# Kernel optimization log

Measured on AMD Instinct MI355X. Metric: run time of the kernel, lower is better.

The kernel has to match this reference:

```python
import jax, jax.numpy as jnp
import numpy as np
from jax import lax

NUM_CLASSES = 21      # VOC: background (class 0) + 20 fg classes
TOP_K = 200           # max detections kept per (image, class)
CONF_THRESH = 0.01
NMS_THRESH = 0.45
VAR0, VAR1 = 0.1, 0.2 # cfg.VARIANCE
K_PRE = 256           # candidates pre-selected per class before NMS (fixed-shape NMS)


def setup_inputs() -> dict:
    key = jax.random.key(0)
    k1, k2, k3 = jax.random.split(key, 3)
    B, P, C = 32, 8732, NUM_CLASSES
    loc_data = jax.random.normal(k1, (B, P, 4), dtype=jnp.float32)
    conf_data = jax.random.normal(k2, (B, P, C), dtype=jnp.float32)
    u = jax.random.uniform(k3, (P, 4), dtype=jnp.float32)
    # priors in center-offset form: centers in [0,1), w/h in [0.02, 0.32)
    prior_data = jnp.concatenate([u[:, :2], 0.02 + 0.3 * u[:, 2:]], axis=-1)
    return {"loc_data": loc_data, "conf_data": conf_data, "prior_data": prior_data}


def decode(loc, priors):
    # loc, priors: [..., 4]; priors are (cx, cy, w, h)
    centers = priors[..., :2] + loc[..., :2] * VAR0 * priors[..., 2:]
    wh = priors[..., 2:] * jnp.exp(loc[..., 2:] * VAR1)
    xy_min = centers - wh * 0.5
    return jnp.concatenate([xy_min, xy_min + wh], axis=-1)  # (x1,y1,x2,y2)


def pairwise_iou(b):
    # b: [K, 4] corner boxes -> [K, K] IoU
    area = jnp.maximum(b[:, 2] - b[:, 0], 0.0) * jnp.maximum(b[:, 3] - b[:, 1], 0.0)
    lt = jnp.maximum(b[:, None, :2], b[None, :, :2])
    rb = jnp.minimum(b[:, None, 2:], b[None, :, 2:])
    wh = jnp.clip(rb - lt, 0.0)
    inter = wh[..., 0] * wh[..., 1]
    union = area[:, None] + area[None, :] - inter
    return inter / jnp.maximum(union, 1e-9)


def nms_one_class(scores_p, boxes_p4):
    # scores_p: [P], boxes_p4: [P, 4]; fixed-shape NMS -> [TOP_K, 5] (score, x1, y1, x2, y2)
    vals, idx = lax.top_k(scores_p, K_PRE)          # sorted descending
    cand = boxes_p4[idx]                            # [K_PRE, 4]
    valid = vals > CONF_THRESH
    iou = pairwise_iou(cand)                        # [K_PRE, K_PRE]
    ar = jnp.arange(K_PRE)

    def step(keep, i):
        # a kept box suppresses later boxes overlapping it above threshold
        sup = keep[i] & (iou[i] > NMS_THRESH) & (ar > i)
        return keep & (~sup), None

    keep, _ = lax.scan(step, valid, ar)
    kept_scores = jnp.where(keep, vals, 0.0)
    # kept entries are already score-ordered; pull the top TOP_K survivors to the front
    sv, si = lax.top_k(kept_scores, TOP_K)
    out_boxes = jnp.where(sv[:, None] > 0.0, cand[si], 0.0)
    return jnp.concatenate([sv[:, None], out_boxes], axis=-1)  # [TOP_K, 5]


def reference(loc_data, conf_data, prior_data):
    # loc_data: [B, P, 4], conf_data: [B, P, C], prior_data: [P, 4]
    probs = jax.nn.softmax(conf_data, axis=-1)                     # [B, P, C]
    probs_fg = jnp.swapaxes(probs[..., 1:], 1, 2)                  # [B, C-1, P] (skip background)
    boxes = decode(loc_data, prior_data[None, :, :])               # [B, P, 4]
    # vmap over classes, then over batch
    per_class = jax.vmap(nms_one_class, in_axes=(0, None))         # ([C-1,P],[P,4]) -> [C-1,TOP_K,5]
    per_image = jax.vmap(per_class, in_axes=(0, 0))
    return per_image(probs_fg, boxes)                              # [B, C-1, TOP_K, 5]
```

## Files before the change

kernel.cpp:

```cpp
#include <hip/hip_runtime.h>
#include <stdint.h>

typedef unsigned long long ull;

#define NUM_CLASSES 21
#define NFG 20
#define TOPK 200
#define KPRE 256
#define CONF_TH 0.01f
#define NMS_TH 0.45f
#define VAR0 0.1f
#define VAR1 0.2f
#define NVMAX 35
#define BITS_CONF 0x3C23D70Au
#define BITS_ONE1 0x3F800001u
#define BSLOT(g) ((g) + ((g) >> 6))

__global__ __launch_bounds__(256) void softmax_probs_kernel(
    const float* __restrict__ conf, float* __restrict__ probs, int P) {
    __shared__ __align__(16) float buf[256 * NUM_CLASSES];
    __shared__ __align__(16) float obuf[NFG * 256];
    const int t = threadIdx.x;
    const int b = blockIdx.y;
    const int p0 = blockIdx.x << 8;
    const int cnt = min(256, P - p0);
    const float* src = conf + ((size_t)b * P + p0) * NUM_CLASSES;

    if (cnt == 256) {
        const float4* s4 = (const float4*)src;
        float4* b4 = (float4*)buf;
#pragma unroll
        for (int k = 0; k < 6; ++k) {
            int i = (k << 8) + t;
            if (i < (256 * NUM_CLASSES) / 4) b4[i] = s4[i];
        }
    } else {
        int n = cnt * NUM_CLASSES;
        for (int i = t; i < n; i += 256) buf[i] = src[i];
    }
    __syncthreads();

    if (t < cnt) {
        const float* row = buf + t * NUM_CLASSES;
        float x[NUM_CLASSES];
        float mx = row[0];
        x[0] = mx;
#pragma unroll
        for (int j = 1; j < NUM_CLASSES; ++j) { x[j] = row[j]; mx = fmaxf(mx, x[j]); }
        float s = 0.f;
#pragma unroll
        for (int j = 0; j < NUM_CLASSES; ++j) { x[j] = expf(x[j] - mx); s += x[j]; }
#pragma unroll
        for (int c = 1; c < NUM_CLASSES; ++c)
            obuf[(c - 1) * 256 + t] = x[c] / s;
    }
    __syncthreads();

    float* dst = probs + ((size_t)b * NFG) * P + p0;
    if (cnt == 256) {
#pragma unroll
        for (int k = 0; k < 5; ++k) {
            int e = (k << 8) + t;
            int c = e >> 6;
            int f = e & 63;
            float4 val = ((const float4*)obuf)[(c << 6) + f];
            *(float4*)(dst + (size_t)c * P + (f << 2)) = val;
        }
    } else {
        for (int e = t; e < NFG * cnt; e += 256) {
            int c = e / cnt;
            int f = e - c * cnt;
            dst[(size_t)c * P + f] = obuf[c * 256 + f];
        }
    }
}

__global__ __launch_bounds__(KPRE) void nms_topk_kernel(
    const float* __restrict__ probs, const float* __restrict__ loc,
    const float* __restrict__ prior, float* __restrict__ out, int B, int P) {

    __shared__ ull arr[2 * KPRE];
    __shared__ ull arr2[2 * KPRE];
    __shared__ int wsum[2][4];
    __shared__ int s_cnt;
    __shared__ float4 sbox[KPRE + (KPRE >> 6)];
    __shared__ float sarea[KPRE + (KPRE >> 6)];
    __shared__ ull smask[KPRE][5];
    __shared__ ull kept_mask[4];

    const int t = threadIdx.x;
    const int lane = t & 63;
    const int wid = t >> 6;
    const ull lmask_lt = (1ULL << lane) - 1ULL;
    const int pair = blockIdx.x;
    const int b = pair / NFG;
    const float* sp = probs + (size_t)pair * P;

    unsigned int ubits[NVMAX];
#pragma unroll
    for (int i = 0; i < NVMAX; ++i) {
        int p = (i << 8) + t;
        ubits[i] = (p < P) ? __float_as_uint(sp[p]) : 0u;
    }

    {
        unsigned int lo = BITS_CONF, hi = BITS_ONE1;
        while (hi - lo > 1u) {
            unsigned int mid = lo + ((hi - lo) >> 1);
            int c = 0;
#pragma unroll
            for (int i = 0; i < NVMAX; ++i)
                c += __popcll(__ballot(ubits[i] >= mid));
            if (c >= KPRE / 4) lo = mid; else hi = mid;
        }
        if (lane == 0) wsum[0][wid] = (int)lo;
    }
    __syncthreads();
    unsigned int T = (unsigned int)min(min(wsum[0][0], wsum[0][1]),
                                       min(wsum[0][2], wsum[0][3]));

    int nval;
    for (int attempt = 0;; ++attempt) {
        if (t == 0) s_cnt = 0;
        __syncthreads();
        int wtot = 0;
#pragma unroll
        for (int i = 0; i < NVMAX; ++i) {
            int p = (i << 8) + t;
            bool pred = (p < P) && (ubits[i] >= T);
            wtot += __popcll(__ballot(pred));
        }
        int wbase = 0;
        if (lane == 0) wbase = atomicAdd(&s_cnt, wtot);
        wbase = __shfl(wbase, 0);
        int run = wbase;
#pragma unroll
        for (int i = 0; i < NVMAX; ++i) {
            int p = (i << 8) + t;
            bool pred = (p < P) && (ubits[i] >= T);
            ull bal = __ballot(pred);
            if (pred) {
                int slot = run + __popcll(bal & lmask_lt);
                if (slot < 2 * KPRE)
                    arr[slot] = ((ull)ubits[i] << 32) | (unsigned int)(~p);
            }
            run += __popcll(bal);
        }
        __syncthreads();
        if (s_cnt <= 2 * KPRE || attempt == 1) { nval = min(s_cnt, 2 * KPRE); break; }
        unsigned int lo = T, hi = BITS_ONE1;
        int it = 0;
        while (hi - lo > 1u) {
            unsigned int mid = lo + ((hi - lo) >> 1);
            int c = 0;
#pragma unroll
            for (int i = 0; i < NVMAX; ++i)
                c += __popcll(__ballot(ubits[i] >= mid));
            if (lane == 0) wsum[it & 1][wid] = c;
            __syncthreads();
            int totc = wsum[it & 1][0] + wsum[it & 1][1] + wsum[it & 1][2] + wsum[it & 1][3];
            if (totc >= KPRE) lo = mid; else hi = mid;
            ++it;
        }
        T = lo;
    }

    for (int e = t; e < 2 * KPRE; e += KPRE)
        if (e >= nval) arr[e] = 0ULL;
    __syncthreads();

    ull k0 = arr[t];
    ull k1 = arr[t + KPRE];
    {
        int lstage = 0;
#pragma unroll
        for (int kk = 2; kk <= 2 * KPRE; kk <<= 1) {
#pragma unroll
            for (int j = kk >> 1; j > 0; j >>= 1) {
                if (j == KPRE) {
                    ull mx = (k0 > k1) ? k0 : k1;
                    ull mn = (k0 > k1) ? k1 : k0;
                    k0 = mx; k1 = mn;
                } else if (j >= 64) {
                    ull* A = (lstage & 1) ? arr : arr2;
                    ++lstage;
                    A[t] = k0; A[t + KPRE] = k1;
                    __syncthreads();
                    ull o0 = A[t ^ j];
                    ull o1 = A[(t + KPRE) ^ j];
                    bool amLow = ((t & j) == 0);
                    bool d0 = ((t & kk) == 0);
                    bool d1 = (((t + KPRE) & kk) == 0);
                    k0 = (d0 == amLow) ? ((k0 > o0) ? k0 : o0) : ((k0 > o0) ? o0 : k0);
                    k1 = (d1 == amLow) ? ((k1 > o1) ? k1 : o1) : ((k1 > o1) ? o1 : k1);
                } else {
                    ull o0 = __shfl_xor(k0, j);
                    ull o1 = __shfl_xor(k1, j);
                    bool amLow = ((t & j) == 0);
                    bool d0 = ((t & kk) == 0);
                    bool d1 = (((t + KPRE) & kk) == 0);
                    k0 = (d0 == amLow) ? ((k0 > o0) ? k0 : o0) : ((k0 > o0) ? o0 : k0);
                    k1 = (d1 == amLow) ? ((k1 > o1) ? k1 : o1) : ((k1 > o1) ? o1 : k1);
                }
            }
        }
    }
    const ull key = k0;

    float v = __uint_as_float((unsigned int)(key >> 32));
    int idx = (int)(~(unsigned int)(key & 0xFFFFFFFFu));
    if (idx < 0 || idx >= P) { idx = 0; v = 0.f; }

    const float4 lv = *(const float4*)(loc + ((size_t)b * P + idx) * 4);
    const float4 pv = *(const float4*)(prior + (size_t)idx * 4);
    float cx = pv.x + (lv.x * VAR0) * pv.z;
    float cy = pv.y + (lv.y * VAR0) * pv.w;
    float w = pv.z * expf(lv.z * VAR1);
    float h = pv.w * expf(lv.w * VAR1);
    float x1 = cx - w * 0.5f;
    float y1 = cy - h * 0.5f;
    float x2 = x1 + w;
    float y2 = y1 + h;
    float myarea = fmaxf(x2 - x1, 0.f) * fmaxf(y2 - y1, 0.f);

    sbox[BSLOT(t)] = make_float4(x1, y1, x2, y2);
    sarea[BSLOT(t)] = myarea;
    __syncthreads();

#pragma unroll
    for (int rep = 0; rep < 3; ++rep) {
        int pid = t + (rep << 8);
        if (pid < 640) {
            int r, w2;
            if (pid < 64)       { r = pid;                w2 = 0; }
            else if (pid < 192) { int q = pid - 64;  r = 64  + (q >> 1); w2 = q & 1; }
            else if (pid < 384) { int q = pid - 192; int q3 = q / 3; r = 128 + q3; w2 = q - 3 * q3; }
            else                { int q = pid - 384; r = 192 + (q >> 2); w2 = q & 3; }
            float4 rb = sbox[BSLOT(r)];
            float ra = sarea[BSLOT(r)];
            ull mm = 0ULL;
            for (int i = 0; i < 64; ++i) {
                int g = (w2 << 6) + i;
                float4 gb = sbox[BSLOT(g)];
                float lx = fmaxf(gb.x, rb.x), ly = fmaxf(gb.y, rb.y);
                float rx = fminf(gb.z, rb.z), ry = fminf(gb.w, rb.w);
                float iw = fmaxf(rx - lx, 0.f), ih = fmaxf(ry - ly, 0.f);
                float inter = iw * ih;
                float uni = sarea[BSLOT(g)] + ra - inter;
                bool s = (inter / fmaxf(uni, 1e-9f)) > NMS_TH;
                mm |= ((ull)(s ? 1u : 0u)) << i;
            }
            smask[r][w2] = mm;
        }
    }
    __syncthreads();

    ull m0 = smask[t][0];
    ull m1 = (wid >= 1) ? smask[t][1] : 0ULL;
    ull m2 = (wid >= 2) ? smask[t][2] : 0ULL;
    ull m3 = (wid >= 3) ? smask[t][3] : 0ULL;
    if (wid == 0) m0 &= lmask_lt;
    else if (wid == 1) m1 &= lmask_lt;
    else if (wid == 2) m2 &= lmask_lt;
    else m3 &= lmask_lt;

    int alive = (v > CONF_TH) ? 1 : 0;
    ull mykept = 0ULL;
#pragma unroll
    for (int w2 = 0; w2 < 4; ++w2) {
        if (wid == w2) {
            if (w2 > 0 && (m0 & kept_mask[0])) alive = 0;
            if (w2 > 1 && (m1 & kept_mask[1])) alive = 0;
            if (w2 > 2 && (m2 & kept_mask[2])) alive = 0;
            ull mw = (w2 == 0) ? m0 : (w2 == 1) ? m1 : (w2 == 2) ? m2 : m3;
            ull validb = __ballot(alive != 0);
            ull todo = __ballot((mw & validb) != 0ULL) & validb;
            ull kept = validb & ~todo;
            while (todo) {
                int i = __builtin_ctzll(todo);
                ull row = __shfl(mw, i);
                if ((row & kept) == 0ULL) kept |= (1ULL << i);
                todo &= (todo - 1ULL);
            }
            mykept = kept;
            alive = (int)((kept >> lane) & 1ULL);
            if (lane == 0) kept_mask[w2] = kept;
        }
        __syncthreads();
    }

    int rank = 0;
#pragma unroll
    for (int w2 = 0; w2 < 4; ++w2)
        if (w2 < wid) rank += __popcll(kept_mask[w2]);
    rank += __popcll(mykept & lmask_lt);
    int total = 0;
#pragma unroll
    for (int w2 = 0; w2 < 4; ++w2) total += __popcll(kept_mask[w2]);

    float* orow = out + (size_t)pair * TOPK * 5;
    if (alive && rank < TOPK) {
        float* o = orow + rank * 5;
        o[0] = v; o[1] = x1; o[2] = y1; o[3] = x2; o[4] = y2;
    }
    if (t < TOPK && t >= total) {
        float* o = orow + t * 5;
        o[0] = 0.f; o[1] = 0.f; o[2] = 0.f; o[3] = 0.f; o[4] = 0.f;
    }
}

extern "C" void kernel_launch(void* const* d_in, const int* in_sizes, int n_in,
                              void* d_out, int out_size, void* d_ws, size_t ws_size,
                              hipStream_t stream) {
    const float* loc = (const float*)d_in[0];
    const float* conf = (const float*)d_in[1];
    const float* prior = (const float*)d_in[2];
    float* out = (float*)d_out;
    float* probs = (float*)d_ws;

    int P = in_sizes[2] / 4;
    int B = in_sizes[0] / (4 * P);

    dim3 g1((P + 255) / 256, B);
    softmax_probs_kernel<<<g1, 256, 0, stream>>>(conf, probs, P);
    nms_topk_kernel<<<B * NFG, KPRE, 0, stream>>>(probs, loc, prior, out, B, P);
}
```

Measured before the change: 137.5 us.

## Compute per-row softmax stats only and recompute probabilities inside NMS kernel

Measured after the change: 144.3 us. 1.05x slower.

```diff
diff --git a/kernel.cpp b/kernel.cpp
--- a/kernel.cpp
+++ b/kernel.cpp
@@ -16,10 +16,9 @@
 #define BITS_ONE1 0x3F800001u
 #define BSLOT(g) ((g) + ((g) >> 6))
 
-__global__ __launch_bounds__(256) void softmax_probs_kernel(
-    const float* __restrict__ conf, float* __restrict__ probs, int P) {
+__global__ __launch_bounds__(256) void rownorm_kernel(
+    const float* __restrict__ conf, float2* __restrict__ norm, int P) {
     __shared__ __align__(16) float buf[256 * NUM_CLASSES];
-    __shared__ __align__(16) float obuf[NFG * 256];
     const int t = threadIdx.x;
     const int b = blockIdx.y;
     const int p0 = blockIdx.x << 8;
@@ -49,35 +48,15 @@
         for (int j = 1; j < NUM_CLASSES; ++j) { x[j] = row[j]; mx = fmaxf(mx, x[j]); }
         float s = 0.f;
 #pragma unroll
-        for (int j = 0; j < NUM_CLASSES; ++j) { x[j] = expf(x[j] - mx); s += x[j]; }
-#pragma unroll
-        for (int c = 1; c < NUM_CLASSES; ++c)
-            obuf[(c - 1) * 256 + t] = x[c] / s;
-    }
-    __syncthreads();
-
-    float* dst = probs + ((size_t)b * NFG) * P + p0;
-    if (cnt == 256) {
-#pragma unroll
-        for (int k = 0; k < 5; ++k) {
-            int e = (k << 8) + t;
-            int c = e >> 6;
-            int f = e & 63;
-            float4 val = ((const float4*)obuf)[(c << 6) + f];
-            *(float4*)(dst + (size_t)c * P + (f << 2)) = val;
-        }
-    } else {
-        for (int e = t; e < NFG * cnt; e += 256) {
-            int c = e / cnt;
-            int f = e - c * cnt;
-            dst[(size_t)c * P + f] = obuf[c * 256 + f];
-        }
+        for (int j = 0; j < NUM_CLASSES; ++j) s += expf(x[j] - mx);
+        norm[(size_t)b * P + p0 + t] = make_float2(mx, s);
     }
 }
 
 __global__ __launch_bounds__(KPRE) void nms_topk_kernel(
-    const float* __restrict__ probs, const float* __restrict__ loc,
-    const float* __restrict__ prior, float* __restrict__ out, int B, int P) {
+    const float* __restrict__ conf, const float2* __restrict__ norm,
+    const float* __restrict__ loc, const float* __restrict__ prior,
+    float* __restrict__ out, int B, int P) {
 
     __shared__ ull arr[2 * KPRE];
     __shared__ ull arr2[2 * KPRE];
@@ -92,26 +71,43 @@
     const int lane = t & 63;
     const int wid = t >> 6;
     const ull lmask_lt = (1ULL << lane) - 1ULL;
-    const int pair = blockIdx.x;
-    const int b = pair / NFG;
-    const float* sp = probs + (size_t)pair * P;
+
+    const int g = blockIdx.x;
+    int b, c;
+    if ((B & 7) == 0) {
+        int k = g >> 3;
+        b = ((k / NFG) << 3) + (g & 7);
+        c = k - (k / NFG) * NFG;
+    } else {
+        b = g / NFG;
+        c = g - (g / NFG) * NFG;
+    }
+    const int pair = b * NFG + c;
+    const float* cb = conf + ((size_t)b * P) * NUM_CLASSES + (c + 1);
+    const float2* nb = norm + (size_t)b * P;
 
     unsigned int ubits[NVMAX];
 #pragma unroll
     for (int i = 0; i < NVMAX; ++i) {
         int p = (i << 8) + t;
-        ubits[i] = (p < P) ? __float_as_uint(sp[p]) : 0u;
+        if (p < P) {
+            float x = cb[(size_t)p * NUM_CLASSES];
+            float2 ms = nb[p];
+            ubits[i] = __float_as_uint(expf(x - ms.x) / ms.y);
+        } else {
+            ubits[i] = 0u;
+        }
     }
 
     {
         unsigned int lo = BITS_CONF, hi = BITS_ONE1;
         while (hi - lo > 1u) {
             unsigned int mid = lo + ((hi - lo) >> 1);
-            int c = 0;
+            int cc = 0;
 #pragma unroll
             for (int i = 0; i < NVMAX; ++i)
-                c += __popcll(__ballot(ubits[i] >= mid));
-            if (c >= KPRE / 4) lo = mid; else hi = mid;
+                cc += __popcll(__ballot(ubits[i] >= mid));
+            if (cc >= KPRE / 4) lo = mid; else hi = mid;
         }
         if (lane == 0) wsum[0][wid] = (int)lo;
     }
@@ -152,11 +148,11 @@
         int it = 0;
         while (hi - lo > 1u) {
             unsigned int mid = lo + ((hi - lo) >> 1);
-            int c = 0;
+            int cc = 0;
 #pragma unroll
             for (int i = 0; i < NVMAX; ++i)
-                c += __popcll(__ballot(ubits[i] >= mid));
-            if (lane == 0) wsum[it & 1][wid] = c;
+                cc += __popcll(__ballot(ubits[i] >= mid));
+            if (lane == 0) wsum[it & 1][wid] = cc;
             __syncthreads();
             int totc = wsum[it & 1][0] + wsum[it & 1][1] + wsum[it & 1][2] + wsum[it & 1][3];
             if (totc >= KPRE) lo = mid; else hi = mid;
@@ -240,13 +236,13 @@
             float ra = sarea[BSLOT(r)];
             ull mm = 0ULL;
             for (int i = 0; i < 64; ++i) {
-                int g = (w2 << 6) + i;
-                float4 gb = sbox[BSLOT(g)];
+                int gg = (w2 << 6) + i;
+                float4 gb = sbox[BSLOT(gg)];
                 float lx = fmaxf(gb.x, rb.x), ly = fmaxf(gb.y, rb.y);
                 float rx = fminf(gb.z, rb.z), ry = fminf(gb.w, rb.w);
                 float iw = fmaxf(rx - lx, 0.f), ih = fmaxf(ry - ly, 0.f);
                 float inter = iw * ih;
-                float uni = sarea[BSLOT(g)] + ra - inter;
+                float uni = sarea[BSLOT(gg)] + ra - inter;
                 bool s = (inter / fmaxf(uni, 1e-9f)) > NMS_TH;
                 mm |= ((ull)(s ? 1u : 0u)) << i;
             }
@@ -316,12 +312,12 @@
     const float* conf = (const float*)d_in[1];
     const float* prior = (const float*)d_in[2];
     float* out = (float*)d_out;
-    float* probs = (float*)d_ws;
+    float2* norm = (float2*)d_ws;
 
     int P = in_sizes[2] / 4;
     int B = in_sizes[0] / (4 * P);
 
     dim3 g1((P + 255) / 256, B);
-    softmax_probs_kernel<<<g1, 256, 0, stream>>>(conf, probs, P);
-    nms_topk_kernel<<<B * NFG, KPRE, 0, stream>>>(probs, loc, prior, out, B, P);
+    rownorm_kernel<<<g1, 256, 0, stream>>>(conf, norm, P);
+    nms_topk_kernel<<<B * NFG, KPRE, 0, stream>>>(conf, norm, loc, prior, out, B, P);
 }
```

## Read softmax rows directly from global and remap NMS block-to-pair order

Applied to the files above, without the earlier changes.

Result: no change. 135.3 us (-1.7%).

```diff
diff --git a/kernel.cpp b/kernel.cpp
--- a/kernel.cpp
+++ b/kernel.cpp
@@ -18,30 +18,14 @@
 
 __global__ __launch_bounds__(256) void softmax_probs_kernel(
     const float* __restrict__ conf, float* __restrict__ probs, int P) {
-    __shared__ __align__(16) float buf[256 * NUM_CLASSES];
     __shared__ __align__(16) float obuf[NFG * 256];
     const int t = threadIdx.x;
     const int b = blockIdx.y;
     const int p0 = blockIdx.x << 8;
     const int cnt = min(256, P - p0);
-    const float* src = conf + ((size_t)b * P + p0) * NUM_CLASSES;
-
-    if (cnt == 256) {
-        const float4* s4 = (const float4*)src;
-        float4* b4 = (float4*)buf;
-#pragma unroll
-        for (int k = 0; k < 6; ++k) {
-            int i = (k << 8) + t;
-            if (i < (256 * NUM_CLASSES) / 4) b4[i] = s4[i];
-        }
-    } else {
-        int n = cnt * NUM_CLASSES;
-        for (int i = t; i < n; i += 256) buf[i] = src[i];
-    }
-    __syncthreads();
 
     if (t < cnt) {
-        const float* row = buf + t * NUM_CLASSES;
+        const float* row = conf + ((size_t)b * P + p0 + t) * NUM_CLASSES;
         float x[NUM_CLASSES];
         float mx = row[0];
         x[0] = mx;
@@ -92,8 +76,18 @@
     const int lane = t & 63;
     const int wid = t >> 6;
     const ull lmask_lt = (1ULL << lane) - 1ULL;
-    const int pair = blockIdx.x;
-    const int b = pair / NFG;
+
+    const int g = blockIdx.x;
+    int b, c;
+    if ((B & 7) == 0) {
+        int k = g >> 3;
+        b = ((k / NFG) << 3) + (g & 7);
+        c = k - (k / NFG) * NFG;
+    } else {
+        b = g / NFG;
+        c = g - (g / NFG) * NFG;
+    }
+    const int pair = b * NFG + c;
     const float* sp = probs + (size_t)pair * P;
 
     unsigned int ubits[NVMAX];
@@ -107,11 +101,11 @@
         unsigned int lo = BITS_CONF, hi = BITS_ONE1;
         while (hi - lo > 1u) {
             unsigned int mid = lo + ((hi - lo) >> 1);
-            int c = 0;
+            int cc = 0;
 #pragma unroll
             for (int i = 0; i < NVMAX; ++i)
-                c += __popcll(__ballot(ubits[i] >= mid));
-            if (c >= KPRE / 4) lo = mid; else hi = mid;
+                cc += __popcll(__ballot(ubits[i] >= mid));
+            if (cc >= KPRE / 4) lo = mid; else hi = mid;
         }
         if (lane == 0) wsum[0][wid] = (int)lo;
     }
@@ -152,11 +146,11 @@
         int it = 0;
         while (hi - lo > 1u) {
             unsigned int mid = lo + ((hi - lo) >> 1);
-            int c = 0;
+            int cc = 0;
 #pragma unroll
             for (int i = 0; i < NVMAX; ++i)
-                c += __popcll(__ballot(ubits[i] >= mid));
-            if (lane == 0) wsum[it & 1][wid] = c;
+                cc += __popcll(__ballot(ubits[i] >= mid));
+            if (lane == 0) wsum[it & 1][wid] = cc;
             __syncthreads();
             int totc = wsum[it & 1][0] + wsum[it & 1][1] + wsum[it & 1][2] + wsum[it & 1][3];
             if (totc >= KPRE) lo = mid; else hi = mid;
@@ -240,13 +234,13 @@
             float ra = sarea[BSLOT(r)];
             ull mm = 0ULL;
             for (int i = 0; i < 64; ++i) {
-                int g = (w2 << 6) + i;
-                float4 gb = sbox[BSLOT(g)];
+                int gg = (w2 << 6) + i;
+                float4 gb = sbox[BSLOT(gg)];
                 float lx = fmaxf(gb.x, rb.x), ly = fmaxf(gb.y, rb.y);
                 float rx = fminf(gb.z, rb.z), ry = fminf(gb.w, rb.w);
                 float iw = fmaxf(rx - lx, 0.f), ih = fmaxf(ry - ly, 0.f);
                 float inter = iw * ih;
-                float uni = sarea[BSLOT(g)] + ra - inter;
+                float uni = sarea[BSLOT(gg)] + ra - inter;
                 bool s = (inter / fmaxf(uni, 1e-9f)) > NMS_TH;
                 mm |= ((ull)(s ? 1u : 0u)) << i;
             }
```
